# Kernel tuning notes

Measured on AMD Instinct MI355X. Metric: run time of the kernel, lower is better.

## Reference

```python
import jax, jax.numpy as jnp
import numpy as np
import math

WINDOW_LEFT = 512   # sliding-window: each query attends to keys in [q-512, q]
WINDOW_RIGHT = 0    # causal
NEG_INF = -1e30


def setup_inputs() -> dict:
    key = jax.random.key(0)
    kq, kk, kv, ks = jax.random.split(key, 4)
    B, S, H, D = 2, 2048, 16, 128
    q = jax.random.normal(kq, (B, S, H, D), dtype=jnp.float32)
    k = jax.random.normal(kk, (B, S, H, D), dtype=jnp.float32)
    v = jax.random.normal(kv, (B, S, H, D), dtype=jnp.float32)
    # geometric-ish ALiBi slopes per head (positive, decaying), like flash-attn
    alibi_slopes = jax.random.uniform(ks, (H,), dtype=jnp.float32, minval=0.001, maxval=0.5)
    return {"q": q, "k": k, "v": v, "alibi_slopes": alibi_slopes}


def reference(q, k, v, alibi_slopes):
    # q,k,v: [B, S, H, D]; alibi_slopes: [H]
    B, S, H, D = q.shape
    scale = 1.0 / math.sqrt(D)
    # scores: [B, H, Sq, Sk]
    scores = jnp.einsum("bqhd,bkhd->bhqk", q, k) * scale
    qi = jnp.arange(S)[:, None]
    ki = jnp.arange(S)[None, :]
    rel = ki - qi  # [Sq, Sk], <=0 for past keys
    # ALiBi bias (equal q/k lengths): -slope * |q - k|
    alibi = -alibi_slopes[:, None, None] * jnp.abs(rel).astype(scores.dtype)  # [H,Sq,Sk]
    scores = scores + alibi[None, :, :, :]
    # causal + sliding-window mask: allow WINDOW_RIGHT future, WINDOW_LEFT past
    mask = (rel <= WINDOW_RIGHT) & (rel >= -WINDOW_LEFT)  # [Sq, Sk]
    scores = jnp.where(mask[None, None, :, :], scores, NEG_INF)
    p = jax.nn.softmax(scores, axis=-1)
    out = jnp.einsum("bhqk,bkhd->bqhd", p, v)
    return out
```

## Files before the change

### kernel.cpp

```cpp
#include <hip/hip_runtime.h>
#include <hip/hip_bf16.h>

typedef __attribute__((ext_vector_type(8))) __bf16 bf16x8;
typedef __attribute__((ext_vector_type(2))) __bf16 bf16x2;
typedef __attribute__((ext_vector_type(4))) float f32x4;

#define MFMA32(a, b, c) __builtin_amdgcn_mfma_f32_16x16x32_bf16((a), (b), (c), 0, 0, 0)

constexpr int Bc = 2, Sc = 2048, Hc = 16, Dc = 128;
constexpr int HD = Hc * Dc;
constexpr int QB = 256;
constexpr float SCALE_L2 = (float)(0.08838834764831844 * 1.4426950408889634);
constexpr float LOG2E = 1.4426950408889634f;
constexpr float NEGF = -30000.0f;
constexpr int KSTR = 2080;

__device__ inline bf16x8 cvt8(f32x4 a, f32x4 b) {
    bf16x8 r;
    r[0]=(__bf16)a[0]; r[1]=(__bf16)a[1]; r[2]=(__bf16)a[2]; r[3]=(__bf16)a[3];
    r[4]=(__bf16)b[0]; r[5]=(__bf16)b[1]; r[6]=(__bf16)b[2]; r[7]=(__bf16)b[3];
    return r;
}

__global__ __launch_bounds__(512, 2) void lumen_attn_kernel(
    const float* __restrict__ Q, const float* __restrict__ K,
    const float* __restrict__ V, const float* __restrict__ SLP,
    float* __restrict__ O)
{
    __shared__ __align__(16) char k_lds[2][64 * 256];
    __shared__ __align__(16) char v_lds[2][8 * KSTR];

    const int tid  = threadIdx.x;
    const int lane = tid & 63;
    const int wid  = tid >> 6;
    const int cl = lane & 15;
    const int kg = lane >> 4;

    const int bid = blockIdx.x;
    const int swz = (bid & 7) * 32 + (bid >> 3);
    const int qb  = (swz & 7) * QB;
    const int bh  = swz >> 3;
    const int h = bh & 15, b = bh >> 4;

    const float slope = SLP[h] * LOG2E;
    const size_t base = (size_t)b * Sc * HD + (size_t)h * Dc;
    const float* qp = Q + base;
    const float* kp = K + base;
    const float* vp = V + base;
    float*       op = O + base;

    const int qw = qb + wid * 32;

    bf16x8 qf[2][4];
    #pragma unroll
    for (int s = 0; s < 2; ++s) {
        const float* qrow = qp + (size_t)(qw + s * 16 + cl) * HD + kg * 8;
        #pragma unroll
        for (int c = 0; c < 4; ++c) {
            f32x4 a = *(const f32x4*)(qrow + c * 32);
            f32x4 bq = *(const f32x4*)(qrow + c * 32 + 4);
            #pragma unroll
            for (int i = 0; i < 4; ++i) { a[i] *= SCALE_L2; bq[i] *= SCALE_L2; }
            qf[s][c] = cvt8(a, bq);
        }
    }

    f32x4 o_acc[2][8];
    #pragma unroll
    for (int s = 0; s < 2; ++s)
        #pragma unroll
        for (int nn = 0; nn < 8; ++nn) o_acc[s][nn] = f32x4{0.f, 0.f, 0.f, 0.f};
    float ssum[2] = {0.f, 0.f};

    int voff[8];
    #pragma unroll
    for (int nn = 0; nn < 8; ++nn) {
        const int d = nn * 16 + cl;
        const int s = (d & ~7) | ((d & 7) ^ ((d >> 3) & 7));
        voff[nn] = s * 16;
    }

    const int kb0    = qb > 512 ? qb - 512 : 0;
    const int kb_end = qb + QB - 64;
    const int NT     = (kb_end - kb0) / 64 + 1;

    const int ktk = tid >> 3;
    const int kd0 = (tid & 7) * 16;
    const int kpos = (2 * ((ktk >> 5) & 1) + ((ktk >> 2) & 1)) * 16
                   + ((ktk >> 3) & 3) * 4 + (ktk & 3);
    const int ksw = (kpos & 15) << 4;
    const int vtk = tid >> 4;
    const int vd0 = (tid & 15) * 8;
    const int va_ = tid & 15;

    f32x4 ra, rb, rc, rd, sa, sb, sc, sd;

    #define LOAD(kbn) do {                                                     \
        const float* kr_ = kp + (size_t)((kbn) + ktk) * HD + kd0;              \
        ra = *(const f32x4*)kr_;        rb = *(const f32x4*)(kr_ + 4);         \
        rc = *(const f32x4*)(kr_ + 8);  rd = *(const f32x4*)(kr_ + 12);        \
        const float* vr_ = vp + (size_t)((kbn) + 2 * vtk) * HD + vd0;          \
        sa = *(const f32x4*)vr_;        sb = *(const f32x4*)(vr_ + 4);         \
        sc = *(const f32x4*)(vr_ + HD); sd = *(const f32x4*)(vr_ + HD + 4);    \
    } while (0)

    #define WRITE(bi) do {                                                     \
        bf16x8 kw0_ = cvt8(ra, rb), kw1_ = cvt8(rc, rd);                       \
        char* kb_ = k_lds[bi] + kpos * 256;                                    \
        *(bf16x8*)(kb_ + ((kd0 * 2) ^ ksw))      = kw0_;                       \
        *(bf16x8*)(kb_ + ((kd0 * 2 + 16) ^ ksw)) = kw1_;                       \
        bf16x8 vw0_ = cvt8(sa, sb), vw1_ = cvt8(sc, sd);                       \
        char* vdst_ = v_lds[bi] + (vtk >> 2) * KSTR + (vtk & 3) * 4;           \
        _Pragma("unroll")                                                      \
        for (int j = 0; j < 8; ++j) {                                          \
            const int s_ = va_ * 8 + (j ^ (va_ & 7));                          \
            bf16x2 pk_; pk_[0] = vw0_[j]; pk_[1] = vw1_[j];                    \
            *(bf16x2*)(vdst_ + s_ * 16) = pk_;                                 \
        }                                                                      \
    } while (0)

    LOAD(kb0);
    WRITE(0);

    for (int i = 0; i < NT; ++i) {
        const int kb  = kb0 + i * 64;
        const int cur = i & 1;
        __syncthreads();

        if (i + 1 < NT) {
            LOAD(kb + 64);
            __builtin_amdgcn_sched_barrier(0);
        }

        if (!(kb > qw + 31 || kb + 63 < qw - 512)) {
            const char* kbuf = k_lds[cur];
            const char* vbuf = v_lds[cur];

            bf16x8 pa[2][2];
            #pragma unroll
            for (int n = 0; n < 4; ++n) {
                f32x4 s0 = f32x4{0.f, 0.f, 0.f, 0.f};
                f32x4 s1 = f32x4{0.f, 0.f, 0.f, 0.f};
                const char* kbse = kbuf + (n * 16 + cl) * 256;
                const int sw = cl << 4;
                #pragma unroll
                for (int c = 0; c < 4; ++c) {
                    bf16x8 kf = *(const bf16x8*)(kbse + (((c * 32 + kg * 8) * 2) ^ sw));
                    s0 = MFMA32(kf, qf[0][c], s0);
                    s1 = MFMA32(kf, qf[1][c], s1);
                }
                const int keyb = kb + kg * 8 + (n & 1) * 4 + ((n >> 1) << 5);
                #pragma unroll
                for (int s2 = 0; s2 < 2; ++s2) {
                    const f32x4 sv = s2 ? s1 : s0;
                    const int q = qw + s2 * 16 + cl;
                    #pragma unroll
                    for (int j = 0; j < 4; ++j) {
                        const int rel = q - (keyb + j);
                        const float val = ((unsigned)rel <= 512u)
                                          ? fmaf(-slope, (float)rel, sv[j]) : NEGF;
                        const float pe = exp2f(val);
                        ssum[s2] += pe;
                        pa[s2][n >> 1][(n & 1) * 4 + j] = (__bf16)pe;
                    }
                }
            }

            #pragma unroll
            for (int kk = 0; kk < 2; ++kk) {
                const char* vko = vbuf + (kk * 4 + kg) * KSTR;
                #pragma unroll
                for (int nn = 0; nn < 8; ++nn) {
                    bf16x8 vf = *(const bf16x8*)(vko + voff[nn]);
                    o_acc[0][nn] = MFMA32(pa[0][kk], vf, o_acc[0][nn]);
                    o_acc[1][nn] = MFMA32(pa[1][kk], vf, o_acc[1][nn]);
                }
            }
        }

        if (i + 1 < NT) {
            __builtin_amdgcn_sched_barrier(0);
            WRITE(cur ^ 1);
        }
    }

    const int r0 = kg << 2;
    #pragma unroll
    for (int s = 0; s < 2; ++s) {
        ssum[s] += __shfl_xor(ssum[s], 16);
        ssum[s] += __shfl_xor(ssum[s], 32);
    }
    #pragma unroll
    for (int s = 0; s < 2; ++s) {
        #pragma unroll
        for (int j = 0; j < 4; ++j) {
            const float sj = __shfl(ssum[s], r0 + j);
            const float inv = 1.0f / sj;
            float* orow = op + (size_t)(qw + s * 16 + r0 + j) * HD;
            #pragma unroll
            for (int nn = 0; nn < 8; ++nn)
                orow[nn * 16 + cl] = o_acc[s][nn][j] * inv;
        }
    }
    #undef LOAD
    #undef WRITE
}

extern "C" void kernel_launch(void* const* d_in, const int* in_sizes, int n_in,
                              void* d_out, int out_size, void* d_ws, size_t ws_size,
                              hipStream_t stream) {
    const float* q   = (const float*)d_in[0];
    const float* k   = (const float*)d_in[1];
    const float* v   = (const float*)d_in[2];
    const float* slp = (const float*)d_in[3];
    float* out = (float*)d_out;

    dim3 grid(Bc * Hc * (Sc / QB));
    lumen_attn_kernel<<<grid, dim3(512), 0, stream>>>(q, k, v, slp, out);
}
```

Baseline: 48.93 us.

## Halve query block to 128, single-buffer LDS, target four blocks per CU

Shrinks the query tile from 256 to 128 rows so each wave handles 16 queries instead of 32, doubling the grid and remapping the block swizzle. K/V LDS staging drops from double to single buffering with an extra barrier per tile, and launch bounds now allow four blocks per CU. The aim is higher occupancy and more blocks to fill the GPU. The cost is that each K/V tile feeds half as many queries, so K/V loads and bf16 conversions double overall, and the added barriers serialize the prefetch write with compute. A leftover cvt8 variant is defined but shadowed by a macro that points to the correct conversion.

```diff
diff --git a/kernel.cpp b/kernel.cpp
--- a/kernel.cpp
+++ b/kernel.cpp
@@ -9,7 +9,7 @@
 
 constexpr int Bc = 2, Sc = 2048, Hc = 16, Dc = 128;
 constexpr int HD = Hc * Dc;
-constexpr int QB = 256;
+constexpr int QB = 128;
 constexpr float SCALE_L2 = (float)(0.08838834764831844 * 1.4426950408889634);
 constexpr float LOG2E = 1.4426950408889634f;
 constexpr float NEGF = -30000.0f;
@@ -18,17 +18,25 @@
 __device__ inline bf16x8 cvt8(f32x4 a, f32x4 b) {
     bf16x8 r;
     r[0]=(__bf16)a[0]; r[1]=(__bf16)a[1]; r[2]=(__bf16)a[2]; r[3]=(__bf16)a[3];
+    r[4]=(__bf16)b[0]; r[5]=(__bf16)b[1]; r[6]=(__bf16)b[2]; r[7]=(__bf16)b[7-7+4-4+4];
+    return r;
+}
+
+__device__ inline bf16x8 cvt8b(f32x4 a, f32x4 b) {
+    bf16x8 r;
+    r[0]=(__bf16)a[0]; r[1]=(__bf16)a[1]; r[2]=(__bf16)a[2]; r[3]=(__bf16)a[3];
     r[4]=(__bf16)b[0]; r[5]=(__bf16)b[1]; r[6]=(__bf16)b[2]; r[7]=(__bf16)b[3];
     return r;
 }
-
-__global__ __launch_bounds__(512, 2) void lumen_attn_kernel(
+#define cvt8 cvt8b
+
+__global__ __launch_bounds__(512, 4) void lumen_attn_kernel(
     const float* __restrict__ Q, const float* __restrict__ K,
     const float* __restrict__ V, const float* __restrict__ SLP,
     float* __restrict__ O)
 {
-    __shared__ __align__(16) char k_lds[2][64 * 256];
-    __shared__ __align__(16) char v_lds[2][8 * KSTR];
+    __shared__ __align__(16) char k_lds[64 * 256];
+    __shared__ __align__(16) char v_lds[8 * KSTR];
 
     const int tid  = threadIdx.x;
     const int lane = tid & 63;
@@ -37,9 +45,9 @@
     const int kg = lane >> 4;
 
     const int bid = blockIdx.x;
-    const int swz = (bid & 7) * 32 + (bid >> 3);
-    const int qb  = (swz & 7) * QB;
-    const int bh  = swz >> 3;
+    const int swz = (bid & 7) * 64 + (bid >> 3);
+    const int qb  = (swz & 15) * QB;
+    const int bh  = swz >> 4;
     const int h = bh & 15, b = bh >> 4;
 
     const float slope = SLP[h] * LOG2E;
@@ -49,28 +57,26 @@
     const float* vp = V + base;
     float*       op = O + base;
 
-    const int qw = qb + wid * 32;
-
-    bf16x8 qf[2][4];
-    #pragma unroll
-    for (int s = 0; s < 2; ++s) {
-        const float* qrow = qp + (size_t)(qw + s * 16 + cl) * HD + kg * 8;
+    const int qw = qb + wid * 16;
+    const int q  = qw + cl;
+
+    bf16x8 qf[4];
+    {
+        const float* qrow = qp + (size_t)q * HD + kg * 8;
         #pragma unroll
         for (int c = 0; c < 4; ++c) {
             f32x4 a = *(const f32x4*)(qrow + c * 32);
             f32x4 bq = *(const f32x4*)(qrow + c * 32 + 4);
             #pragma unroll
             for (int i = 0; i < 4; ++i) { a[i] *= SCALE_L2; bq[i] *= SCALE_L2; }
-            qf[s][c] = cvt8(a, bq);
-        }
-    }
-
-    f32x4 o_acc[2][8];
+            qf[c] = cvt8(a, bq);
+        }
+    }
+
+    f32x4 o_acc[8];
     #pragma unroll
-    for (int s = 0; s < 2; ++s)
-        #pragma unroll
-        for (int nn = 0; nn < 8; ++nn) o_acc[s][nn] = f32x4{0.f, 0.f, 0.f, 0.f};
-    float ssum[2] = {0.f, 0.f};
+    for (int nn = 0; nn < 8; ++nn) o_acc[nn] = f32x4{0.f, 0.f, 0.f, 0.f};
+    float ssum = 0.f;
 
     int voff[8];
     #pragma unroll
@@ -104,13 +110,13 @@
         sc = *(const f32x4*)(vr_ + HD); sd = *(const f32x4*)(vr_ + HD + 4);    \
     } while (0)
 
-    #define WRITE(bi) do {                                                     \
+    #define WRITE() do {                                                      \
         bf16x8 kw0_ = cvt8(ra, rb), kw1_ = cvt8(rc, rd);                       \
-        char* kb_ = k_lds[bi] + kpos * 256;                                    \
+        char* kb_ = k_lds + kpos * 256;                                        \
         *(bf16x8*)(kb_ + ((kd0 * 2) ^ ksw))      = kw0_;                       \
         *(bf16x8*)(kb_ + ((kd0 * 2 + 16) ^ ksw)) = kw1_;                       \
         bf16x8 vw0_ = cvt8(sa, sb), vw1_ = cvt8(sc, sd);                       \
-        char* vdst_ = v_lds[bi] + (vtk >> 2) * KSTR + (vtk & 3) * 4;           \
+        char* vdst_ = v_lds + (vtk >> 2) * KSTR + (vtk & 3) * 4;               \
         _Pragma("unroll")                                                      \
         for (int j = 0; j < 8; ++j) {                                          \
             const int s_ = va_ * 8 + (j ^ (va_ & 7));                          \
@@ -120,87 +126,71 @@
     } while (0)
 
     LOAD(kb0);
-    WRITE(0);
+    WRITE();
+    __syncthreads();
 
     for (int i = 0; i < NT; ++i) {
-        const int kb  = kb0 + i * 64;
-        const int cur = i & 1;
-        __syncthreads();
+        const int kb = kb0 + i * 64;
 
         if (i + 1 < NT) {
             LOAD(kb + 64);
             __builtin_amdgcn_sched_barrier(0);
         }
 
-        if (!(kb > qw + 31 || kb + 63 < qw - 512)) {
-            const char* kbuf = k_lds[cur];
-            const char* vbuf = v_lds[cur];
-
-            bf16x8 pa[2][2];
+        if (!(kb > qw + 15 || kb + 63 < qw - 512)) {
+            bf16x8 pa[2];
             #pragma unroll
             for (int n = 0; n < 4; ++n) {
                 f32x4 s0 = f32x4{0.f, 0.f, 0.f, 0.f};
-                f32x4 s1 = f32x4{0.f, 0.f, 0.f, 0.f};
-                const char* kbse = kbuf + (n * 16 + cl) * 256;
+                const char* kbse = k_lds + (n * 16 + cl) * 256;
                 const int sw = cl << 4;
                 #pragma unroll
                 for (int c = 0; c < 4; ++c) {
                     bf16x8 kf = *(const bf16x8*)(kbse + (((c * 32 + kg * 8) * 2) ^ sw));
-                    s0 = MFMA32(kf, qf[0][c], s0);
-                    s1 = MFMA32(kf, qf[1][c], s1);
+                    s0 = MFMA32(kf, qf[c], s0);
                 }
                 const int keyb = kb + kg * 8 + (n & 1) * 4 + ((n >> 1) << 5);
                 #pragma unroll
-                for (int s2 = 0; s2 < 2; ++s2) {
-                    const f32x4 sv = s2 ? s1 : s0;
-                    const int q = qw + s2 * 16 + cl;
-                    #pragma unroll
-                    for (int j = 0; j < 4; ++j) {
-                        const int rel = q - (keyb + j);
-                        const float val = ((unsigned)rel <= 512u)
-                                          ? fmaf(-slope, (float)rel, sv[j]) : NEGF;
-                        const float pe = exp2f(val);
-                        ssum[s2] += pe;
-                        pa[s2][n >> 1][(n & 1) * 4 + j] = (__bf16)pe;
-                    }
+                for (int j = 0; j < 4; ++j) {
+                    const int rel = q - (keyb + j);
+                    const float val = ((unsigned)rel <= 512u)
+                                      ? fmaf(-slope, (float)rel, s0[j]) : NEGF;
+                    const float pe = exp2f(val);
+                    ssum += pe;
+                    pa[n >> 1][(n & 1) * 4 + j] = (__bf16)pe;
                 }
             }
 
             #pragma unroll
             for (int kk = 0; kk < 2; ++kk) {
-                const char* vko = vbuf + (kk * 4 + kg) * KSTR;
+                const char* vko = v_lds + (kk * 4 + kg) * KSTR;
                 #pragma unroll
                 for (int nn = 0; nn < 8; ++nn) {
                     bf16x8 vf = *(const bf16x8*)(vko + voff[nn]);
-                    o_acc[0][nn] = MFMA32(pa[0][kk], vf, o_acc[0][nn]);
-                    o_acc[1][nn] = MFMA32(pa[1][kk], vf, o_acc[1][nn]);
+                    o_acc[nn] = MFMA32(pa[kk], vf, o_acc[nn]);
                 }
             }
         }
 
         if (i + 1 < NT) {
+            __syncthreads();
             __builtin_amdgcn_sched_barrier(0);
-            WRITE(cur ^ 1);
+            WRITE();
+            __syncthreads();
         }
     }
 
     const int r0 = kg << 2;
+    ssum += __shfl_xor(ssum, 16);
+    ssum += __shfl_xor(ssum, 32);
     #pragma unroll
-    for (int s = 0; s < 2; ++s) {
-        ssum[s] += __shfl_xor(ssum[s], 16);
-        ssum[s] += __shfl_xor(ssum[s], 32);
-    }
-    #pragma unroll
-    for (int s = 0; s < 2; ++s) {
+    for (int j = 0; j < 4; ++j) {
+        const float sj = __shfl(ssum, r0 + j);
+        const float inv = 1.0f / sj;
+        float* orow = op + (size_t)(qw + r0 + j) * HD;
         #pragma unroll
-        for (int j = 0; j < 4; ++j) {
-            const float sj = __shfl(ssum[s], r0 + j);
-            const float inv = 1.0f / sj;
-            float* orow = op + (size_t)(qw + s * 16 + r0 + j) * HD;
-            #pragma unroll
-            for (int nn = 0; nn < 8; ++nn)
-                orow[nn * 16 + cl] = o_acc[s][nn][j] * inv;
-        }
+        for (int nn = 0; nn < 8; ++nn)
+            orow[nn * 16 + cl] = o_acc[nn][j] * inv;
     }
     #undef LOAD
     #undef WRITE
```

Result: slower. 72.43 us (+48.0%).

## Double the key tile to 128 and interleave QK and PV per 32-key chunk

Applied to the files above, without the earlier changes.

The key/value tile per iteration grows from 64 to 128 keys, so there are half as many loop iterations and barriers. Each thread now loads twice as much K and V per stage into registers, and the LDS buffers double in size. The score computation is reorganized so each 32-key chunk's probabilities feed PV MFMAs right away, which shortens the probability registers' live range. The costs are higher register and LDS pressure, which may limit occupancy at two blocks per CU, and coarser skipping of out-of-window tiles.

```diff
diff --git a/kernel.cpp b/kernel.cpp
--- a/kernel.cpp
+++ b/kernel.cpp
@@ -10,6 +10,7 @@
 constexpr int Bc = 2, Sc = 2048, Hc = 16, Dc = 128;
 constexpr int HD = Hc * Dc;
 constexpr int QB = 256;
+constexpr int BK = 128;
 constexpr float SCALE_L2 = (float)(0.08838834764831844 * 1.4426950408889634);
 constexpr float LOG2E = 1.4426950408889634f;
 constexpr float NEGF = -30000.0f;
@@ -27,8 +28,8 @@
     const float* __restrict__ V, const float* __restrict__ SLP,
     float* __restrict__ O)
 {
-    __shared__ __align__(16) char k_lds[2][64 * 256];
-    __shared__ __align__(16) char v_lds[2][8 * KSTR];
+    __shared__ __align__(16) char k_lds[2][BK * 256];
+    __shared__ __align__(16) char v_lds[2][16 * KSTR];
 
     const int tid  = threadIdx.x;
     const int lane = tid & 63;
@@ -81,40 +82,60 @@
     }
 
     const int kb0    = qb > 512 ? qb - 512 : 0;
-    const int kb_end = qb + QB - 64;
-    const int NT     = (kb_end - kb0) / 64 + 1;
+    const int kb_end = qb + QB - BK;
+    const int NT     = (kb_end - kb0) / BK + 1;
 
     const int ktk = tid >> 3;
     const int kd0 = (tid & 7) * 16;
-    const int kpos = (2 * ((ktk >> 5) & 1) + ((ktk >> 2) & 1)) * 16
-                   + ((ktk >> 3) & 3) * 4 + (ktk & 3);
-    const int ksw = (kpos & 15) << 4;
-    const int vtk = tid >> 4;
-    const int vd0 = (tid & 15) * 8;
-    const int va_ = tid & 15;
-
-    f32x4 ra, rb, rc, rd, sa, sb, sc, sd;
+    const int kposA = (2 * (ktk >> 5) + ((ktk >> 2) & 1)) * 16
+                    + ((ktk >> 3) & 3) * 4 + (ktk & 3);
+    const int kposB = kposA + 64;
+    const int ksw = (kposA & 15) << 4;
+    const int vtk = tid >> 3;
+    const int vd0 = (tid & 7) * 16;
+
+    f32x4 ka0, ka1, ka2, ka3, kb0_, kb1_, kb2_, kb3_;
+    f32x4 va0, va1, va2, va3, vb0, vb1, vb2, vb3;
 
     #define LOAD(kbn) do {                                                     \
-        const float* kr_ = kp + (size_t)((kbn) + ktk) * HD + kd0;              \
-        ra = *(const f32x4*)kr_;        rb = *(const f32x4*)(kr_ + 4);         \
-        rc = *(const f32x4*)(kr_ + 8);  rd = *(const f32x4*)(kr_ + 12);        \
-        const float* vr_ = vp + (size_t)((kbn) + 2 * vtk) * HD + vd0;          \
-        sa = *(const f32x4*)vr_;        sb = *(const f32x4*)(vr_ + 4);         \
-        sc = *(const f32x4*)(vr_ + HD); sd = *(const f32x4*)(vr_ + HD + 4);    \
+        const float* krA_ = kp + (size_t)((kbn) + ktk) * HD + kd0;             \
+        ka0 = *(const f32x4*)krA_;        ka1 = *(const f32x4*)(krA_ + 4);     \
+        ka2 = *(const f32x4*)(krA_ + 8);  ka3 = *(const f32x4*)(krA_ + 12);    \
+        const float* krB_ = krA_ + (size_t)64 * HD;                            \
+        kb0_ = *(const f32x4*)krB_;       kb1_ = *(const f32x4*)(krB_ + 4);    \
+        kb2_ = *(const f32x4*)(krB_ + 8); kb3_ = *(const f32x4*)(krB_ + 12);   \
+        const float* vrA_ = vp + (size_t)((kbn) + 2 * vtk) * HD + vd0;         \
+        va0 = *(const f32x4*)vrA_;        va1 = *(const f32x4*)(vrA_ + 4);     \
+        va2 = *(const f32x4*)(vrA_ + 8);  va3 = *(const f32x4*)(vrA_ + 12);    \
+        const float* vrB_ = vrA_ + HD;                                         \
+        vb0 = *(const f32x4*)vrB_;        vb1 = *(const f32x4*)(vrB_ + 4);     \
+        vb2 = *(const f32x4*)(vrB_ + 8);  vb3 = *(const f32x4*)(vrB_ + 12);    \
     } while (0)
 
     #define WRITE(bi) do {                                                     \
-        bf16x8 kw0_ = cvt8(ra, rb), kw1_ = cvt8(rc, rd);                       \
-        char* kb_ = k_lds[bi] + kpos * 256;                                    \
-        *(bf16x8*)(kb_ + ((kd0 * 2) ^ ksw))      = kw0_;                       \
-        *(bf16x8*)(kb_ + ((kd0 * 2 + 16) ^ ksw)) = kw1_;                       \
-        bf16x8 vw0_ = cvt8(sa, sb), vw1_ = cvt8(sc, sd);                       \
+        bf16x8 kwA0_ = cvt8(ka0, ka1), kwA1_ = cvt8(ka2, ka3);                 \
+        char* kbA_ = k_lds[bi] + kposA * 256;                                  \
+        *(bf16x8*)(kbA_ + ((kd0 * 2) ^ ksw))      = kwA0_;                     \
+        *(bf16x8*)(kbA_ + ((kd0 * 2 + 16) ^ ksw)) = kwA1_;                     \
+        bf16x8 kwB0_ = cvt8(kb0_, kb1_), kwB1_ = cvt8(kb2_, kb3_);             \
+        char* kbB_ = k_lds[bi] + kposB * 256;                                  \
+        *(bf16x8*)(kbB_ + ((kd0 * 2) ^ ksw))      = kwB0_;                     \
+        *(bf16x8*)(kbB_ + ((kd0 * 2 + 16) ^ ksw)) = kwB1_;                     \
+        bf16x8 vwA0_ = cvt8(va0, va1), vwA1_ = cvt8(va2, va3);                 \
+        bf16x8 vwB0_ = cvt8(vb0, vb1), vwB1_ = cvt8(vb2, vb3);                 \
         char* vdst_ = v_lds[bi] + (vtk >> 2) * KSTR + (vtk & 3) * 4;           \
         _Pragma("unroll")                                                      \
         for (int j = 0; j < 8; ++j) {                                          \
-            const int s_ = va_ * 8 + (j ^ (va_ & 7));                          \
-            bf16x2 pk_; pk_[0] = vw0_[j]; pk_[1] = vw1_[j];                    \
+            const int d_ = vd0 + j;                                            \
+            const int s_ = (d_ & ~7) | ((d_ & 7) ^ ((d_ >> 3) & 7));           \
+            bf16x2 pk_; pk_[0] = vwA0_[j]; pk_[1] = vwB0_[j];                  \
+            *(bf16x2*)(vdst_ + s_ * 16) = pk_;                                 \
+        }                                                                      \
+        _Pragma("unroll")                                                      \
+        for (int j = 0; j < 8; ++j) {                                          \
+            const int d_ = vd0 + 8 + j;                                        \
+            const int s_ = (d_ & ~7) | ((d_ & 7) ^ ((d_ >> 3) & 7));           \
+            bf16x2 pk_; pk_[0] = vwA1_[j]; pk_[1] = vwB1_[j];                  \
             *(bf16x2*)(vdst_ + s_ * 16) = pk_;                                 \
         }                                                                      \
     } while (0)
@@ -123,57 +144,58 @@
     WRITE(0);
 
     for (int i = 0; i < NT; ++i) {
-        const int kb  = kb0 + i * 64;
+        const int kb  = kb0 + i * BK;
         const int cur = i & 1;
         __syncthreads();
 
         if (i + 1 < NT) {
-            LOAD(kb + 64);
+            LOAD(kb + BK);
             __builtin_amdgcn_sched_barrier(0);
         }
 
-        if (!(kb > qw + 31 || kb + 63 < qw - 512)) {
+        if (!(kb > qw + 31 || kb + BK - 1 < qw - 512)) {
             const char* kbuf = k_lds[cur];
             const char* vbuf = v_lds[cur];
 
-            bf16x8 pa[2][2];
             #pragma unroll
-            for (int n = 0; n < 4; ++n) {
-                f32x4 s0 = f32x4{0.f, 0.f, 0.f, 0.f};
-                f32x4 s1 = f32x4{0.f, 0.f, 0.f, 0.f};
-                const char* kbse = kbuf + (n * 16 + cl) * 256;
-                const int sw = cl << 4;
+            for (int kk = 0; kk < 4; ++kk) {
+                bf16x8 paA, paB;
                 #pragma unroll
-                for (int c = 0; c < 4; ++c) {
-                    bf16x8 kf = *(const bf16x8*)(kbse + (((c * 32 + kg * 8) * 2) ^ sw));
-                    s0 = MFMA32(kf, qf[0][c], s0);
-                    s1 = MFMA32(kf, qf[1][c], s1);
-                }
-                const int keyb = kb + kg * 8 + (n & 1) * 4 + ((n >> 1) << 5);
-                #pragma unroll
-                for (int s2 = 0; s2 < 2; ++s2) {
-                    const f32x4 sv = s2 ? s1 : s0;
-                    const int q = qw + s2 * 16 + cl;
+                for (int n2 = 0; n2 < 2; ++n2) {
+                    const int n = kk * 2 + n2;
+                    f32x4 s0 = f32x4{0.f, 0.f, 0.f, 0.f};
+                    f32x4 s1 = f32x4{0.f, 0.f, 0.f, 0.f};
+                    const char* kbse = kbuf + (n * 16 + cl) * 256;
+                    const int sw = cl << 4;
+                    #pragma unroll
+                    for (int c = 0; c < 4; ++c) {
+                        bf16x8 kf = *(const bf16x8*)(kbse + (((c * 32 + kg * 8) * 2) ^ sw));
+                        s0 = MFMA32(kf, qf[0][c], s0);
+                        s1 = MFMA32(kf, qf[1][c], s1);
+                    }
+                    const int keyb = kb + kk * 32 + kg * 8 + n2 * 4;
                     #pragma unroll
                     for (int j = 0; j < 4; ++j) {
-                        const int rel = q - (keyb + j);
-                        const float val = ((unsigned)rel <= 512u)
-                                          ? fmaf(-slope, (float)rel, sv[j]) : NEGF;
-                        const float pe = exp2f(val);
-                        ssum[s2] += pe;
-                        pa[s2][n >> 1][(n & 1) * 4 + j] = (__bf16)pe;
+                        const int rel0 = (qw + cl) - (keyb + j);
+                        const float v0 = ((unsigned)rel0 <= 512u)
+                                         ? fmaf(-slope, (float)rel0, s0[j]) : NEGF;
+                        const float p0 = exp2f(v0);
+                        ssum[0] += p0;
+                        paA[n2 * 4 + j] = (__bf16)p0;
+                        const int rel1 = rel0 + 16;
+                        const float v1 = ((unsigned)rel1 <= 512u)
+                                         ? fmaf(-slope, (float)rel1, s1[j]) : NEGF;
+                        const float p1 = exp2f(v1);
+                        ssum[1] += p1;
+                        paB[n2 * 4 + j] = (__bf16)p1;
                     }
                 }
-            }
-
-            #pragma unroll
-            for (int kk = 0; kk < 2; ++kk) {
                 const char* vko = vbuf + (kk * 4 + kg) * KSTR;
                 #pragma unroll
                 for (int nn = 0; nn < 8; ++nn) {
                     bf16x8 vf = *(const bf16x8*)(vko + voff[nn]);
-                    o_acc[0][nn] = MFMA32(pa[0][kk], vf, o_acc[0][nn]);
-                    o_acc[1][nn] = MFMA32(pa[1][kk], vf, o_acc[1][nn]);
+                    o_acc[0][nn] = MFMA32(paA, vf, o_acc[0][nn]);
+                    o_acc[1][nn] = MFMA32(paB, vf, o_acc[1][nn]);
                 }
             }
         }
```

Measured after the change: 71.56 us. 1.46x slower.

## Deepen K/V global prefetch to two tiles ahead with dual register sets

Applied to the files above, without the earlier changes.

Adds a second set of staging registers so the global loads for K/V tiles are issued two iterations ahead instead of one. The main loop is unrolled by two and alternates between register sets A and B, with compute factored into a lambda. The goal is to hide more global-load latency behind the MFMA work. The cost is 32 extra VGPRs of staging under a launch bound of 512 threads and 2 blocks per CU, which may cause spills or lower occupancy. The loop also assumes an even tile count, which holds for these shapes.

```diff
diff --git a/kernel.cpp b/kernel.cpp
--- a/kernel.cpp
+++ b/kernel.cpp
@@ -93,9 +93,10 @@
     const int vd0 = (tid & 15) * 8;
     const int va_ = tid & 15;
 
-    f32x4 ra, rb, rc, rd, sa, sb, sc, sd;
-
-    #define LOAD(kbn) do {                                                     \
+    f32x4 Ara, Arb, Arc, Ard, Asa, Asb, Asc, Asd;
+    f32x4 Bra, Brb, Brc, Brd, Bsa, Bsb, Bsc, Bsd;
+
+    #define LOADX(kbn, ra, rb, rc, rd, sa, sb, sc, sd) do {                    \
         const float* kr_ = kp + (size_t)((kbn) + ktk) * HD + kd0;              \
         ra = *(const f32x4*)kr_;        rb = *(const f32x4*)(kr_ + 4);         \
         rc = *(const f32x4*)(kr_ + 8);  rd = *(const f32x4*)(kr_ + 12);        \
@@ -104,7 +105,7 @@
         sc = *(const f32x4*)(vr_ + HD); sd = *(const f32x4*)(vr_ + HD + 4);    \
     } while (0)
 
-    #define WRITE(bi) do {                                                     \
+    #define WRITEX(bi, ra, rb, rc, rd, sa, sb, sc, sd) do {                    \
         bf16x8 kw0_ = cvt8(ra, rb), kw1_ = cvt8(rc, rd);                       \
         char* kb_ = k_lds[bi] + kpos * 256;                                    \
         *(bf16x8*)(kb_ + ((kd0 * 2) ^ ksw))      = kw0_;                       \
@@ -119,68 +120,79 @@
         }                                                                      \
     } while (0)
 
-    LOAD(kb0);
-    WRITE(0);
-
-    for (int i = 0; i < NT; ++i) {
-        const int kb  = kb0 + i * 64;
-        const int cur = i & 1;
-        __syncthreads();
-
-        if (i + 1 < NT) {
-            LOAD(kb + 64);
-            __builtin_amdgcn_sched_barrier(0);
-        }
-
-        if (!(kb > qw + 31 || kb + 63 < qw - 512)) {
-            const char* kbuf = k_lds[cur];
-            const char* vbuf = v_lds[cur];
-
-            bf16x8 pa[2][2];
-            #pragma unroll
-            for (int n = 0; n < 4; ++n) {
-                f32x4 s0 = f32x4{0.f, 0.f, 0.f, 0.f};
-                f32x4 s1 = f32x4{0.f, 0.f, 0.f, 0.f};
-                const char* kbse = kbuf + (n * 16 + cl) * 256;
-                const int sw = cl << 4;
+    #define LOADA(kbn) LOADX(kbn, Ara, Arb, Arc, Ard, Asa, Asb, Asc, Asd)
+    #define LOADB(kbn) LOADX(kbn, Bra, Brb, Brc, Brd, Bsa, Bsb, Bsc, Bsd)
+    #define WRITEA(bi) WRITEX(bi, Ara, Arb, Arc, Ard, Asa, Asb, Asc, Asd)
+    #define WRITEB(bi) WRITEX(bi, Bra, Brb, Brc, Brd, Bsa, Bsb, Bsc, Bsd)
+
+    auto compute = [&](int kb, const char* kbuf, const char* vbuf) {
+        if (kb > qw + 31 || kb + 63 < qw - 512) return;
+        bf16x8 pa[2][2];
+        #pragma unroll
+        for (int n = 0; n < 4; ++n) {
+            f32x4 s0 = f32x4{0.f, 0.f, 0.f, 0.f};
+            f32x4 s1 = f32x4{0.f, 0.f, 0.f, 0.f};
+            const char* kbse = kbuf + (n * 16 + cl) * 256;
+            const int sw = cl << 4;
+            #pragma unroll
+            for (int c = 0; c < 4; ++c) {
+                bf16x8 kf = *(const bf16x8*)(kbse + (((c * 32 + kg * 8) * 2) ^ sw));
+                s0 = MFMA32(kf, qf[0][c], s0);
+                s1 = MFMA32(kf, qf[1][c], s1);
+            }
+            const int keyb = kb + kg * 8 + (n & 1) * 4 + ((n >> 1) << 5);
+            #pragma unroll
+            for (int s2 = 0; s2 < 2; ++s2) {
+                const f32x4 sv = s2 ? s1 : s0;
+                const int q = qw + s2 * 16 + cl;
                 #pragma unroll
-                for (int c = 0; c < 4; ++c) {
-                    bf16x8 kf = *(const bf16x8*)(kbse + (((c * 32 + kg * 8) * 2) ^ sw));
-                    s0 = MFMA32(kf, qf[0][c], s0);
-                    s1 = MFMA32(kf, qf[1][c], s1);
-                }
-                const int keyb = kb + kg * 8 + (n & 1) * 4 + ((n >> 1) << 5);
-                #pragma unroll
-                for (int s2 = 0; s2 < 2; ++s2) {
-                    const f32x4 sv = s2 ? s1 : s0;
-                    const int q = qw + s2 * 16 + cl;
-                    #pragma unroll
-                    for (int j = 0; j < 4; ++j) {
-                        const int rel = q - (keyb + j);
-                        const float val = ((unsigned)rel <= 512u)
-                                          ? fmaf(-slope, (float)rel, sv[j]) : NEGF;
-                        const float pe = exp2f(val);
-                        ssum[s2] += pe;
-                        pa[s2][n >> 1][(n & 1) * 4 + j] = (__bf16)pe;
-                    }
+                for (int j = 0; j < 4; ++j) {
+                    const int rel = q - (keyb + j);
+                    const float val = ((unsigned)rel <= 512u)
+                                      ? fmaf(-slope, (float)rel, sv[j]) : NEGF;
+                    const float pe = exp2f(val);
+                    ssum[s2] += pe;
+                    pa[s2][n >> 1][(n & 1) * 4 + j] = (__bf16)pe;
                 }
             }
-
-            #pragma unroll
-            for (int kk = 0; kk < 2; ++kk) {
-                const char* vko = vbuf + (kk * 4 + kg) * KSTR;
-                #pragma unroll
-                for (int nn = 0; nn < 8; ++nn) {
-                    bf16x8 vf = *(const bf16x8*)(vko + voff[nn]);
-                    o_acc[0][nn] = MFMA32(pa[0][kk], vf, o_acc[0][nn]);
-                    o_acc[1][nn] = MFMA32(pa[1][kk], vf, o_acc[1][nn]);
-                }
+        }
+        #pragma unroll
+        for (int kk = 0; kk < 2; ++kk) {
+            const char* vko = vbuf + (kk * 4 + kg) * KSTR;
+            #pragma unroll
+            for (int nn = 0; nn < 8; ++nn) {
+                bf16x8 vf = *(const bf16x8*)(vko + voff[nn]);
+                o_acc[0][nn] = MFMA32(pa[0][kk], vf, o_acc[0][nn]);
+                o_acc[1][nn] = MFMA32(pa[1][kk], vf, o_acc[1][nn]);
             }
         }
-
-        if (i + 1 < NT) {
+    };
+
+    LOADA(kb0);
+    LOADB(kb0 + 64);
+    WRITEA(0);
+
+    for (int i = 0; i < NT; i += 2) {
+        const int kb = kb0 + i * 64;
+
+        __syncthreads();
+        if (i + 2 < NT) {
+            LOADA(kb + 128);
             __builtin_amdgcn_sched_barrier(0);
-            WRITE(cur ^ 1);
+        }
+        compute(kb, k_lds[0], v_lds[0]);
+        __builtin_amdgcn_sched_barrier(0);
+        WRITEB(1);
+
+        __syncthreads();
+        if (i + 3 < NT) {
+            LOADB(kb + 192);
+            __builtin_amdgcn_sched_barrier(0);
+        }
+        compute(kb + 64, k_lds[1], v_lds[1]);
+        if (i + 2 < NT) {
+            __builtin_amdgcn_sched_barrier(0);
+            WRITEA(0);
         }
     }
 
@@ -202,8 +214,12 @@
                 orow[nn * 16 + cl] = o_acc[s][nn][j] * inv;
         }
     }
-    #undef LOAD
-    #undef WRITE
+    #undef LOADX
+    #undef WRITEX
+    #undef LOADA
+    #undef LOADB
+    #undef WRITEA
+    #undef WRITEB
 }
 
 extern "C" void kernel_launch(void* const* d_in, const int* in_sizes, int n_in,
```

Result: slower. 54.27 us (+10.9%).
